# Optimization experiments

Measured on AMD Instinct MI355X. Metric: run time of the kernel, lower is better.

## Reference

```python
import jax, jax.numpy as jnp
import numpy as np

N = 100000       # nodes
E0 = 1600000     # edges without self loops
E = E0 + N       # with self loops appended (attr 0), matching add_self_loops
DIN = 128        # input_dim
HID = 64         # nb_hidden_gnn (per-head out_channels)
HEADS = 4
EMB = 128
L = 3            # nb_layer
NEG_SLOPE = 0.2
BN_EPS = 1e-5


def setup_inputs() -> dict:
    key = jax.random.key(0)
    ks = jax.random.split(key, 12)
    # edges with no self loops; self loops (i,i) appended with edge_attr 0
    row = jax.random.randint(ks[0], (E0,), 0, N)
    off = jax.random.randint(ks[1], (E0,), 1, N)
    col = (row + off) % N
    loops = jnp.arange(N, dtype=row.dtype)
    edge_index = jnp.stack([jnp.concatenate([row, loops]),
                            jnp.concatenate([col, loops])])
    edge_attr = jnp.concatenate([jax.random.normal(ks[2], (E0, 1), jnp.float32),
                                 jnp.zeros((N, 1), jnp.float32)])
    x = jax.random.normal(ks[3], (N, DIN), jnp.float32)
    HC = HEADS * HID
    linN0 = jax.random.normal(ks[4], (DIN, HC)) * HC ** -0.5
    linN_rest = jax.random.normal(ks[5], (L - 1, HID, HC)) * HC ** -0.5
    linE_all = jax.random.normal(ks[6], (L, 1, HEADS)) * HEADS ** -0.5  # nb_edge_attr=1
    att_all = jax.random.normal(ks[7], (L, HEADS, 2 * HID + 1)) * (2 * HID + 1) ** -0.5
    bias_all = jnp.zeros((L, HID))  # concat=False -> bias [out_channels]
    bn_gamma = jnp.ones((L - 1, HID))
    bn_beta = jnp.zeros((L - 1, HID))
    W = jax.random.normal(ks[8], (HID, EMB)) * HID ** -0.5
    b = jnp.zeros((EMB,))
    return {"x": x, "edge_index": edge_index, "edge_attr": edge_attr,
            "linN0": linN0, "linN_rest": linN_rest, "linE_all": linE_all,
            "att_all": att_all, "bias_all": bias_all,
            "bn_gamma": bn_gamma, "bn_beta": bn_beta, "W": W, "b": b}


def _gcn_layer(x, row, col, edge_attr, linN, linE, att, bias, bn):
    n = x.shape[0]
    if bn is not None:
        gamma, beta = bn
        mu = x.mean(axis=0)
        var = x.var(axis=0)
        x = (x - mu) * jax.lax.rsqrt(var + BN_EPS) * gamma + beta
    h = (x @ linN).reshape(n, HEADS, HID)                 # [N,H,C]
    e = (edge_attr @ linE)                                # [E,H] (nb_edge_attr=1)
    att_i = att[:, :HID]                                  # [H,C]
    att_j = att[:, HID:2 * HID]                           # [H,C]
    att_e = att[:, 2 * HID:]                              # [H,1]
    # per-node partial scores avoid gathering full features twice
    s_i = jnp.einsum('nhc,hc->nh', h, att_i)
    s_j = jnp.einsum('nhc,hc->nh', h, att_j)
    logits = s_i[row] + s_j[col] + e * att_e[:, 0]        # [E,H]
    logits = jax.nn.leaky_relu(logits, NEG_SLOPE)
    # segment softmax over destination nodes (edge_index[1])
    m = jax.ops.segment_max(logits, col, num_segments=n)
    p = jnp.exp(logits - m[col])
    denom = jax.ops.segment_sum(p, col, num_segments=n)
    alpha = p / (denom[col] + 1e-16)
    # message: alpha * x[source], scatter-add to destination
    msg = alpha[:, :, None] * h[row]                      # [E,H,C]
    out = jax.ops.segment_sum(msg, col, num_segments=n)   # [N,H,C]
    out = out.mean(axis=1) + bias + h.mean(axis=1)        # concat=False, res=True
    return jax.nn.relu(out)


def reference(x, edge_index, edge_attr, linN0, linN_rest, linE_all, att_all,
              bias_all, bn_gamma, bn_beta, W, b):
    row, col = edge_index[0], edge_index[1]
    emb = x
    for l in range(L):
        linN = linN0 if l == 0 else linN_rest[l - 1]
        bn = None if l == 0 else (bn_gamma[l - 1], bn_beta[l - 1])
        emb = _gcn_layer(emb, row, col, edge_attr, linN, linE_all[l],
                         att_all[l], bias_all[l], bn)
    return emb @ W + b
```

## Files before the change

### kernel.cpp

```cpp
#include <hip/hip_runtime.h>
#include <math.h>

#define NN 100000
#define E0E 1600000
#define EE (E0E + NN)
#define NEG 0.2f
#define BNEPS 1e-5f
#define LOG2E 1.4426950408889634f

typedef float f4 __attribute__((ext_vector_type(4)));
typedef float f2 __attribute__((ext_vector_type(2)));
typedef short s8v __attribute__((ext_vector_type(8)));

__device__ __forceinline__ float wred_max(float v) {
#pragma unroll
  for (int m = 1; m < 64; m <<= 1) v = fmaxf(v, __shfl_xor(v, m, 64));
  return v;
}
__device__ __forceinline__ float wred_sum(float v) {
#pragma unroll
  for (int m = 1; m < 64; m <<= 1) v += __shfl_xor(v, m, 64);
  return v;
}
__device__ __forceinline__ float sel4(float a0, float a1, float a2, float a3, int hd) {
  return (hd & 2) ? ((hd & 1) ? a3 : a2) : ((hd & 1) ? a1 : a0);
}
__device__ __forceinline__ unsigned short f2bf(float x) {
  unsigned u = __float_as_uint(x);
  return (unsigned short)((u + 0x7fffu + ((u >> 16) & 1u)) >> 16);
}
__device__ __forceinline__ float bf2f(unsigned short s) {
  return __uint_as_float(((unsigned)s) << 16);
}

__global__ void k_zero_i32(int* p, int n) {
  int i = blockIdx.x * blockDim.x + threadIdx.x;
  if (i < n) p[i] = 0;
}
__global__ void k_zero_f64(double* p, int n) {
  int i = blockIdx.x * blockDim.x + threadIdx.x;
  if (i < n) p[i] = 0.0;
}
__global__ void k_count(const int* __restrict__ col, int* cnt, int e) {
  int i = blockIdx.x * blockDim.x + threadIdx.x;
  if (i < e) atomicAdd(&cnt[col[i]], 1);
}
#define SCAN_T 1024
__global__ void k_scan1(const int* __restrict__ cnt, int* partial, int n, int chunk) {
  int i = blockIdx.x * blockDim.x + threadIdx.x;
  int beg = i * chunk, end = min(n, beg + chunk);
  int s = 0;
  for (int j = beg; j < end; ++j) s += cnt[j];
  partial[i] = s;
}
__global__ void k_scan2(int* partial) {
  __shared__ int lds[SCAN_T];
  int t = threadIdx.x;
  int v = partial[t];
  lds[t] = v;
  __syncthreads();
  for (int off = 1; off < SCAN_T; off <<= 1) {
    int add = (t >= off) ? lds[t - off] : 0;
    __syncthreads();
    lds[t] += add;
    __syncthreads();
  }
  partial[t] = lds[t] - v;
}
__global__ void k_scan3(const int* __restrict__ cnt, const int* __restrict__ partial,
                        int* rowptr, int* cursor, int n, int chunk, int etot) {
  int i = blockIdx.x * blockDim.x + threadIdx.x;
  int beg = i * chunk, end = min(n, beg + chunk);
  int run = partial[i];
  for (int j = beg; j < end; ++j) {
    rowptr[j] = run;
    cursor[j] = run;
    run += cnt[j];
  }
  if (i == SCAN_T - 1) rowptr[n] = etot;
}
__global__ void k_scatter(const int* __restrict__ row, const int* __restrict__ col,
                          const float* __restrict__ ea, int* cursor, int2* csr, int e) {
  int i = blockIdx.x * blockDim.x + threadIdx.x;
  if (i < e) {
    int c = col[i];
    int p = atomicAdd(&cursor[c], 1);
    csr[p] = make_int2(row[i], __float_as_int(ea[i]));
  }
}

__global__ void k_bnstats(const float* __restrict__ x, double* sums, int n) {
  int f = threadIdx.x & 63;
  int rt = (blockIdx.x * blockDim.x + threadIdx.x) >> 6;
  int rstride = (gridDim.x * blockDim.x) >> 6;
  double s = 0.0, q = 0.0;
  for (int r = rt; r < n; r += rstride) {
    double v = (double)x[(size_t)r * 64 + f];
    s += v;
    q += v * v;
  }
  __shared__ double ls[256], lq[256];
  ls[threadIdx.x] = s;
  lq[threadIdx.x] = q;
  __syncthreads();
  if (threadIdx.x < 64) {
    s = ls[threadIdx.x] + ls[threadIdx.x + 64] + ls[threadIdx.x + 128] + ls[threadIdx.x + 192];
    q = lq[threadIdx.x] + lq[threadIdx.x + 64] + lq[threadIdx.x + 128] + lq[threadIdx.x + 192];
    atomicAdd(&sums[f], s);
    atomicAdd(&sums[64 + f], q);
  }
}
__global__ void k_bnfinal(const double* __restrict__ sums, const float* __restrict__ gamma,
                          const float* __restrict__ beta, float* AB, int n) {
  int f = threadIdx.x;
  if (f < 64) {
    double mean = sums[f] / n;
    double var = sums[64 + f] / n - mean * mean;
    float A = gamma[f] * rsqrtf((float)var + BNEPS);
    AB[f] = A;
    AB[64 + f] = beta[f] - (float)mean * A;
  }
}

__global__ void k_prepw(const float* __restrict__ W, const float* __restrict__ AB,
                        const float* __restrict__ bin, unsigned short* __restrict__ Wt,
                        float* __restrict__ cvec, int K, int N, int mode) {
  int n = threadIdx.x;
  if (n >= N) return;
  float c = (mode == 2) ? bin[n] : 0.f;
  for (int k = 0; k < K; ++k) {
    float w = W[k * N + n];
    float a = 1.f, b = 0.f;
    if (mode == 1) { a = AB[k]; b = AB[64 + k]; }
    Wt[n * K + k] = f2bf(a * w);
    c = fmaf(b, w, c);
  }
  cvec[n] = c;
}

template <int K, int CT, bool ATT, bool OB>
__global__ __launch_bounds__(256, 2) void k_gemm(const float* __restrict__ x,
                                                 const unsigned short* __restrict__ Wt,
                                                 const float* __restrict__ cvec,
                                                 const float* __restrict__ att,
                                                 void* __restrict__ houtv,
                                                 float* __restrict__ s_i,
                                                 float* __restrict__ s_j, int n,
                                                 int ntiles) {
  constexpr int KS = K / 32;
  constexpr int ROWB = 2 * K;
  constexpr int CPR = K / 8;
  constexpr int NCOL = 4 * CT * 16;
  __shared__ unsigned char xs[64 * ROWB];
  const int lane = threadIdx.x & 63;
  const int wv = threadIdx.x >> 6;
  const int l15 = lane & 15;
  const int lq = lane >> 4;
  const int colbase = wv * CT * 16;

  s8v wfr[CT][KS];
#pragma unroll
  for (int ct = 0; ct < CT; ++ct)
#pragma unroll
    for (int ks = 0; ks < KS; ++ks)
      wfr[ct][ks] = *(const s8v*)&Wt[(size_t)(colbase + ct * 16 + l15) * K + ks * 32 + lq * 8];
  float cb[CT][4];
#pragma unroll
  for (int ct = 0; ct < CT; ++ct)
#pragma unroll
    for (int r = 0; r < 4; ++r) cb[ct][r] = cvec[colbase + ct * 16 + lq * 4 + r];
  float ati[ATT ? CT : 1][4], atj[ATT ? CT : 1][4];
  if constexpr (ATT) {
    const float* ar = att + wv * 129;
#pragma unroll
    for (int ct = 0; ct < CT; ++ct)
#pragma unroll
      for (int r = 0; r < 4; ++r) {
        int cc = ct * 16 + lq * 4 + r;
        ati[ct][r] = ar[cc];
        atj[ct][r] = ar[64 + cc];
      }
  }

  for (int t = blockIdx.x; t < ntiles; t += gridDim.x) {
    const int row0 = t * 64;
    __syncthreads();
#pragma unroll
    for (int i = 0; i < (64 * CPR) / 256; ++i) {
      int c = threadIdx.x + i * 256;
      int row = c / CPR, kc = c % CPR;
      int rg = min(row0 + row, n - 1);
      const float* xp = x + (size_t)rg * K + kc * 8;
      f4 a0 = *(const f4*)xp;
      f4 a1 = *(const f4*)(xp + 4);
      union { s8v v; unsigned short u[8]; } pk;
      pk.u[0] = f2bf(a0[0]); pk.u[1] = f2bf(a0[1]); pk.u[2] = f2bf(a0[2]); pk.u[3] = f2bf(a0[3]);
      pk.u[4] = f2bf(a1[0]); pk.u[5] = f2bf(a1[1]); pk.u[6] = f2bf(a1[2]); pk.u[7] = f2bf(a1[3]);
      *(s8v*)&xs[row * ROWB + ((kc * 16) ^ ((row & 7) << 4))] = pk.v;
    }
    __syncthreads();
    f4 acc[4][CT];
#pragma unroll
    for (int rt = 0; rt < 4; ++rt)
#pragma unroll
      for (int ct = 0; ct < CT; ++ct) acc[rt][ct] = (f4)0.f;
#pragma unroll
    for (int ks = 0; ks < KS; ++ks) {
      s8v xf[4];
#pragma unroll
      for (int rt = 0; rt < 4; ++rt) {
        int row = rt * 16 + l15;
        int kb = ks * 64 + lq * 16;
        xf[rt] = *(const s8v*)&xs[row * ROWB + (kb ^ ((row & 7) << 4))];
      }
#pragma unroll
      for (int rt = 0; rt < 4; ++rt)
#pragma unroll
        for (int ct = 0; ct < CT; ++ct)
          acc[rt][ct] = __builtin_amdgcn_mfma_f32_16x16x32_bf16(wfr[ct][ks], xf[rt],
                                                                acc[rt][ct], 0, 0, 0);
    }
#pragma unroll
    for (int rt = 0; rt < 4; ++rt) {
      if (row0 + rt * 16 >= n) continue;
      const size_t xrow = (size_t)(row0 + rt * 16 + l15);
      float v[CT][4];
#pragma unroll
      for (int ct = 0; ct < CT; ++ct)
#pragma unroll
        for (int r = 0; r < 4; ++r) v[ct][r] = acc[rt][ct][r] + cb[ct][r];
      if constexpr (OB) {
        float* outp = (float*)houtv;
#pragma unroll
        for (int ct = 0; ct < CT; ++ct) {
          f4 o;
          o[0] = v[ct][0]; o[1] = v[ct][1]; o[2] = v[ct][2]; o[3] = v[ct][3];
          *(f4*)&outp[xrow * NCOL + colbase + ct * 16 + lq * 4] = o;
        }
      } else {
        unsigned short* hout = (unsigned short*)houtv;
#pragma unroll
        for (int ct = 0; ct < CT; ++ct) {
          ushort4 hb4;
          hb4.x = f2bf(v[ct][0]); hb4.y = f2bf(v[ct][1]);
          hb4.z = f2bf(v[ct][2]); hb4.w = f2bf(v[ct][3]);
          *(ushort4*)&hout[xrow * NCOL + colbase + ct * 16 + lq * 4] = hb4;
        }
      }
      if constexpr (ATT) {
        float pi = 0.f, pj = 0.f;
#pragma unroll
        for (int ct = 0; ct < CT; ++ct)
#pragma unroll
          for (int r = 0; r < 4; ++r) {
            pi = fmaf(v[ct][r], ati[ct][r], pi);
            pj = fmaf(v[ct][r], atj[ct][r], pj);
          }
        pi += __shfl_xor(pi, 16, 64); pi += __shfl_xor(pi, 32, 64);
        pj += __shfl_xor(pj, 16, 64); pj += __shfl_xor(pj, 32, 64);
        if (lane < 16) {
          s_i[xrow * 4 + wv] = pi;
          s_j[xrow * 4 + wv] = pj;
        }
      }
    }
  }
}

__global__ __launch_bounds__(256) void k_edge(const int* __restrict__ rowptr,
                                              const int2* __restrict__ csr,
                                              const float* __restrict__ s_i,
                                              const float* __restrict__ s_j,
                                              const unsigned short* __restrict__ hb,
                                              const float* __restrict__ linE,
                                              const float* __restrict__ att,
                                              const float* __restrict__ bias,
                                              float* __restrict__ xout, int n) {
  __shared__ float lp[4][64][4];
  __shared__ int lsrc[4][64];
  const int lane = threadIdx.x & 63;
  const int wid = threadIdx.x >> 6;
  int v = blockIdx.x * 4 + wid;
  if (v >= n) return;
  v = __builtin_amdgcn_readfirstlane(v);
  const int base = rowptr[v];
  const int deg = rowptr[v + 1] - base;

  const float coef0 = linE[0] * att[0 * 129 + 128];
  const float coef1 = linE[1] * att[1 * 129 + 128];
  const float coef2 = linE[2] * att[2 * 129 + 128];
  const float coef3 = linE[3] * att[3 * 129 + 128];
  const float sj0 = s_j[(size_t)v * 4 + 0];
  const float sj1 = s_j[(size_t)v * 4 + 1];
  const float sj2 = s_j[(size_t)v * 4 + 2];
  const float sj3 = s_j[(size_t)v * 4 + 3];

  auto edge_logits = [&](int i, int& src, float& g0, float& g1, float& g2, float& g3) {
    int2 pk = csr[i];
    src = pk.x;
    float ea = __int_as_float(pk.y);
    f4 siv = *(const f4*)&s_i[(size_t)src * 4];
    g0 = siv[0] + sj0 + ea * coef0; g0 = fmaxf(g0, g0 * NEG);
    g1 = siv[1] + sj1 + ea * coef1; g1 = fmaxf(g1, g1 * NEG);
    g2 = siv[2] + sj2 + ea * coef2; g2 = fmaxf(g2, g2 * NEG);
    g3 = siv[3] + sj3 + ea * coef3; g3 = fmaxf(g3, g3 * NEG);
  };

  const int hd = lane >> 4;
  float msel, rdsel;
  bool fast = (deg <= 64);
  if (fast) {
    float g0 = -INFINITY, g1 = -INFINITY, g2 = -INFINITY, g3 = -INFINITY;
    int src = 0;
    bool valid = lane < deg;
    if (valid) edge_logits(base + lane, src, g0, g1, g2, g3);
    float m0 = wred_max(g0), m1 = wred_max(g1), m2 = wred_max(g2), m3 = wred_max(g3);
    float p0 = valid ? exp2f((g0 - m0) * LOG2E) : 0.f;
    float p1 = valid ? exp2f((g1 - m1) * LOG2E) : 0.f;
    float p2 = valid ? exp2f((g2 - m2) * LOG2E) : 0.f;
    float p3 = valid ? exp2f((g3 - m3) * LOG2E) : 0.f;
    if (valid) {
      f4 pp; pp[0] = p0; pp[1] = p1; pp[2] = p2; pp[3] = p3;
      *(f4*)&lp[wid][lane][0] = pp;
      lsrc[wid][lane] = src;
    }
    float d0 = wred_sum(p0), d1 = wred_sum(p1), d2 = wred_sum(p2), d3 = wred_sum(p3);
    rdsel = 1.f / (sel4(d0, d1, d2, d3, hd) + 1e-16f);
    msel = 0.f;
  } else {
    float m0 = -INFINITY, m1 = -INFINITY, m2 = -INFINITY, m3 = -INFINITY;
    for (int c0 = 0; c0 < deg; c0 += 64) {
      int i = c0 + lane;
      if (i < deg) {
        int src; float g0, g1, g2, g3;
        edge_logits(base + i, src, g0, g1, g2, g3);
        m0 = fmaxf(m0, g0); m1 = fmaxf(m1, g1); m2 = fmaxf(m2, g2); m3 = fmaxf(m3, g3);
      }
    }
    m0 = wred_max(m0); m1 = wred_max(m1); m2 = wred_max(m2); m3 = wred_max(m3);
    float d0 = 0, d1 = 0, d2 = 0, d3 = 0;
    for (int c0 = 0; c0 < deg; c0 += 64) {
      int i = c0 + lane;
      if (i < deg) {
        int src; float g0, g1, g2, g3;
        edge_logits(base + i, src, g0, g1, g2, g3);
        d0 += exp2f((g0 - m0) * LOG2E);
        d1 += exp2f((g1 - m1) * LOG2E);
        d2 += exp2f((g2 - m2) * LOG2E);
        d3 += exp2f((g3 - m3) * LOG2E);
      }
    }
    d0 = wred_sum(d0); d1 = wred_sum(d1); d2 = wred_sum(d2); d3 = wred_sum(d3);
    msel = sel4(m0, m1, m2, m3, hd);
    rdsel = 1.f / (sel4(d0, d1, d2, d3, hd) + 1e-16f);
  }

  f4 acc;
  {
    ushort4 hr = *(const ushort4*)&hb[(size_t)v * 256 + lane * 4];
    acc[0] = bf2f(hr.x); acc[1] = bf2f(hr.y); acc[2] = bf2f(hr.z); acc[3] = bf2f(hr.w);
  }
  if (fast) {
    for (int e = 0; e < deg; ++e) {
      int src = lsrc[wid][e];
      float a = lp[wid][e][hd] * rdsel;
      ushort4 hr = *(const ushort4*)&hb[(size_t)src * 256 + lane * 4];
      acc[0] = fmaf(a, bf2f(hr.x), acc[0]);
      acc[1] = fmaf(a, bf2f(hr.y), acc[1]);
      acc[2] = fmaf(a, bf2f(hr.z), acc[2]);
      acc[3] = fmaf(a, bf2f(hr.w), acc[3]);
    }
  } else {
    const float sjsel = sel4(sj0, sj1, sj2, sj3, hd);
    const float cfsel = sel4(coef0, coef1, coef2, coef3, hd);
    for (int e = base; e < base + deg; ++e) {
      int2 pk = csr[e];
      int src = pk.x;
      float ea = __int_as_float(pk.y);
      f4 siv = *(const f4*)&s_i[(size_t)src * 4];
      float lg = sel4(siv[0], siv[1], siv[2], siv[3], hd) + sjsel + ea * cfsel;
      lg = fmaxf(lg, lg * NEG);
      float a = exp2f((lg - msel) * LOG2E) * rdsel;
      ushort4 hr = *(const ushort4*)&hb[(size_t)src * 256 + lane * 4];
      acc[0] = fmaf(a, bf2f(hr.x), acc[0]);
      acc[1] = fmaf(a, bf2f(hr.y), acc[1]);
      acc[2] = fmaf(a, bf2f(hr.z), acc[2]);
      acc[3] = fmaf(a, bf2f(hr.w), acc[3]);
    }
  }
#pragma unroll
  for (int m = 16; m < 64; m <<= 1) {
    acc[0] += __shfl_xor(acc[0], m, 64);
    acc[1] += __shfl_xor(acc[1], m, 64);
    acc[2] += __shfl_xor(acc[2], m, 64);
    acc[3] += __shfl_xor(acc[3], m, 64);
  }
  if (lane < 16) {
    f4 bv = *(const f4*)&bias[lane * 4];
    f4 o;
#pragma unroll
    for (int c = 0; c < 4; ++c) o[c] = fmaxf(acc[c] * 0.25f + bv[c], 0.f);
    *(f4*)&xout[(size_t)v * 64 + lane * 4] = o;
  }
}

extern "C" void kernel_launch(void* const* d_in, const int* in_sizes, int n_in,
                              void* d_out, int out_size, void* d_ws, size_t ws_size,
                              hipStream_t stream) {
  const float* x_in = (const float*)d_in[0];
  const int* ei = (const int*)d_in[1];
  const float* eattr = (const float*)d_in[2];
  const float* linN0 = (const float*)d_in[3];
  const float* linNr = (const float*)d_in[4];
  const float* linE = (const float*)d_in[5];
  const float* attA = (const float*)d_in[6];
  const float* biasA = (const float*)d_in[7];
  const float* bng = (const float*)d_in[8];
  const float* bnb = (const float*)d_in[9];
  const float* W = (const float*)d_in[10];
  const float* bb = (const float*)d_in[11];
  float* out = (float*)d_out;

  const int* row = ei;
  const int* col = ei + EE;

  char* ws = (char*)d_ws;
  size_t o = 0;
  auto alloc = [&](size_t bytes) {
    void* p = ws + o;
    o += (bytes + 255) & ~(size_t)255;
    return p;
  };
  int* cnt = (int*)alloc((size_t)NN * 4);
  int* cursor = (int*)alloc((size_t)NN * 4);
  int* rowptr = (int*)alloc((size_t)(NN + 1) * 4);
  int* partial = (int*)alloc((size_t)SCAN_T * 4);
  int2* csr = (int2*)alloc((size_t)EE * 8);
  unsigned short* h = (unsigned short*)alloc((size_t)NN * 256 * 2);
  float* si = (float*)alloc((size_t)NN * 4 * 4);
  float* sj = (float*)alloc((size_t)NN * 4 * 4);
  float* xa = (float*)alloc((size_t)NN * 64 * 4);
  float* xb = (float*)alloc((size_t)NN * 64 * 4);
  double* bnsum = (double*)alloc(256 * 8);
  float* AB = (float*)alloc(128 * 4);
  unsigned short* Wt = (unsigned short*)alloc((size_t)256 * 128 * 2);
  float* cvec = (float*)alloc(256 * 4);
  if (o > ws_size) return;

  const int chunk = (NN + SCAN_T - 1) / SCAN_T;
  const int NTILES = (NN + 63) / 64;
  const int GG = 521;

  k_zero_i32<<<(NN + 255) / 256, 256, 0, stream>>>(cnt, NN);
  k_zero_f64<<<1, 256, 0, stream>>>(bnsum, 256);
  k_count<<<(EE + 255) / 256, 256, 0, stream>>>(col, cnt, EE);
  k_scan1<<<4, 256, 0, stream>>>(cnt, partial, NN, chunk);
  k_scan2<<<1, SCAN_T, 0, stream>>>(partial);
  k_scan3<<<4, 256, 0, stream>>>(cnt, partial, rowptr, cursor, NN, chunk, EE);
  k_scatter<<<(EE + 255) / 256, 256, 0, stream>>>(row, col, eattr, cursor, csr, EE);

  k_prepw<<<1, 256, 0, stream>>>(linN0, nullptr, nullptr, Wt, cvec, 128, 256, 0);
  k_gemm<128, 4, true, false><<<GG, 256, 0, stream>>>(x_in, Wt, cvec, attA + 0, h, si, sj,
                                                      NN, NTILES);
  k_edge<<<NN / 4, 256, 0, stream>>>(rowptr, csr, si, sj, h, linE + 0, attA + 0, biasA + 0, xa, NN);

  k_bnstats<<<256, 256, 0, stream>>>(xa, bnsum, NN);
  k_bnfinal<<<1, 64, 0, stream>>>(bnsum, bng + 0, bnb + 0, AB, NN);
  k_prepw<<<1, 256, 0, stream>>>(linNr, AB, nullptr, Wt, cvec, 64, 256, 1);
  k_gemm<64, 4, true, false><<<GG, 256, 0, stream>>>(xa, Wt, cvec, attA + 516, h, si, sj,
                                                     NN, NTILES);
  k_edge<<<NN / 4, 256, 0, stream>>>(rowptr, csr, si, sj, h, linE + 4, attA + 516, biasA + 64, xb, NN);

  k_bnstats<<<256, 256, 0, stream>>>(xb, bnsum + 128, NN);
  k_bnfinal<<<1, 64, 0, stream>>>(bnsum + 128, bng + 64, bnb + 64, AB, NN);
  k_prepw<<<1, 256, 0, stream>>>(linNr + 64 * 256, AB, nullptr, Wt, cvec, 64, 256, 1);
  k_gemm<64, 4, true, false><<<GG, 256, 0, stream>>>(xb, Wt, cvec, attA + 2 * 516, h, si, sj,
                                                     NN, NTILES);
  k_edge<<<NN / 4, 256, 0, stream>>>(rowptr, csr, si, sj, h, linE + 8, attA + 2 * 516, biasA + 128, xa, NN);

  k_prepw<<<1, 256, 0, stream>>>(W, nullptr, bb, Wt, cvec, 64, 128, 2);
  k_gemm<64, 2, false, true><<<GG, 256, 0, stream>>>(xa, Wt, cvec, nullptr, out, nullptr,
                                                     nullptr, NN, NTILES);
}
```

Before: 940.1 us.

## Merge init and BN-finalize kernels, unroll edge gather, launch one block per tile

Folds the two zeroing kernels into one init kernel and moves the batch-norm finalize into the weight-prep kernel, dropping three launches per forward. The fast-path message gather in the edge kernel is templated on an unroll factor so several neighbour feature rows are fetched before their FMAs. Each layer uses a different factor (4, 2, 1), which looks like an experiment. GEMM grids now launch one block per 64-row tile instead of a fixed 521 blocks.

```diff
diff --git a/kernel.cpp b/kernel.cpp
--- a/kernel.cpp
+++ b/kernel.cpp
@@ -33,13 +33,10 @@
   return __uint_as_float(((unsigned)s) << 16);
 }
 
-__global__ void k_zero_i32(int* p, int n) {
+__global__ void k_init(int* cnt, double* bnsum, int n) {
   int i = blockIdx.x * blockDim.x + threadIdx.x;
-  if (i < n) p[i] = 0;
-}
-__global__ void k_zero_f64(double* p, int n) {
-  int i = blockIdx.x * blockDim.x + threadIdx.x;
-  if (i < n) p[i] = 0.0;
+  if (i < n) cnt[i] = 0;
+  if (i < 256) bnsum[i] = 0.0;
 }
 __global__ void k_count(const int* __restrict__ col, int* cnt, int e) {
   int i = blockIdx.x * blockDim.x + threadIdx.x;
@@ -110,32 +107,33 @@
     atomicAdd(&sums[64 + f], q);
   }
 }
-__global__ void k_bnfinal(const double* __restrict__ sums, const float* __restrict__ gamma,
-                          const float* __restrict__ beta, float* AB, int n) {
-  int f = threadIdx.x;
-  if (f < 64) {
-    double mean = sums[f] / n;
-    double var = sums[64 + f] / n - mean * mean;
-    float A = gamma[f] * rsqrtf((float)var + BNEPS);
-    AB[f] = A;
-    AB[64 + f] = beta[f] - (float)mean * A;
-  }
-}
-
-__global__ void k_prepw(const float* __restrict__ W, const float* __restrict__ AB,
+
+__global__ void k_prepw(const float* __restrict__ W, const double* __restrict__ bnsum,
+                        const float* __restrict__ gamma, const float* __restrict__ beta,
                         const float* __restrict__ bin, unsigned short* __restrict__ Wt,
                         float* __restrict__ cvec, int K, int N, int mode) {
-  int n = threadIdx.x;
-  if (n >= N) return;
-  float c = (mode == 2) ? bin[n] : 0.f;
+  __shared__ float ABl[128];
+  int t = threadIdx.x;
+  if (mode == 1) {
+    if (t < 64) {
+      double mean = bnsum[t] / NN;
+      double var = bnsum[64 + t] / NN - mean * mean;
+      float A = gamma[t] * rsqrtf((float)var + BNEPS);
+      ABl[t] = A;
+      ABl[64 + t] = beta[t] - (float)mean * A;
+    }
+    __syncthreads();
+  }
+  if (t >= N) return;
+  float c = (mode == 2) ? bin[t] : 0.f;
   for (int k = 0; k < K; ++k) {
-    float w = W[k * N + n];
+    float w = W[k * N + t];
     float a = 1.f, b = 0.f;
-    if (mode == 1) { a = AB[k]; b = AB[64 + k]; }
-    Wt[n * K + k] = f2bf(a * w);
+    if (mode == 1) { a = ABl[k]; b = ABl[64 + k]; }
+    Wt[t * K + k] = f2bf(a * w);
     c = fmaf(b, w, c);
   }
-  cvec[n] = c;
+  cvec[t] = c;
 }
 
 template <int K, int CT, bool ATT, bool OB>
@@ -267,6 +265,7 @@
   }
 }
 
+template <int UNR>
 __global__ __launch_bounds__(256) void k_edge(const int* __restrict__ rowptr,
                                               const int2* __restrict__ csr,
                                               const float* __restrict__ s_i,
@@ -361,14 +360,37 @@
     acc[0] = bf2f(hr.x); acc[1] = bf2f(hr.y); acc[2] = bf2f(hr.z); acc[3] = bf2f(hr.w);
   }
   if (fast) {
-    for (int e = 0; e < deg; ++e) {
-      int src = lsrc[wid][e];
-      float a = lp[wid][e][hd] * rdsel;
-      ushort4 hr = *(const ushort4*)&hb[(size_t)src * 256 + lane * 4];
-      acc[0] = fmaf(a, bf2f(hr.x), acc[0]);
-      acc[1] = fmaf(a, bf2f(hr.y), acc[1]);
-      acc[2] = fmaf(a, bf2f(hr.z), acc[2]);
-      acc[3] = fmaf(a, bf2f(hr.w), acc[3]);
+    int e = 0;
+    if constexpr (UNR > 1) {
+      for (; e + UNR <= deg; e += UNR) {
+        int ss[UNR];
+        float aa[UNR];
+        ushort4 hh[UNR];
+#pragma unroll
+        for (int u = 0; u < UNR; ++u) {
+          ss[u] = lsrc[wid][e + u];
+          aa[u] = lp[wid][e + u][hd] * rdsel;
+        }
+#pragma unroll
+        for (int u = 0; u < UNR; ++u)
+          hh[u] = *(const ushort4*)&hb[(size_t)ss[u] * 256 + lane * 4];
+#pragma unroll
+        for (int u = 0; u < UNR; ++u) {
+          acc[0] = fmaf(aa[u], bf2f(hh[u].x), acc[0]);
+          acc[1] = fmaf(aa[u], bf2f(hh[u].y), acc[1]);
+          acc[2] = fmaf(aa[u], bf2f(hh[u].z), acc[2]);
+          acc[3] = fmaf(aa[u], bf2f(hh[u].w), acc[3]);
+        }
+      }
+    }
+    for (; e < deg; ++e) {
+      int s0 = lsrc[wid][e];
+      float a0 = lp[wid][e][hd] * rdsel;
+      ushort4 h0 = *(const ushort4*)&hb[(size_t)s0 * 256 + lane * 4];
+      acc[0] = fmaf(a0, bf2f(h0.x), acc[0]);
+      acc[1] = fmaf(a0, bf2f(h0.y), acc[1]);
+      acc[2] = fmaf(a0, bf2f(h0.z), acc[2]);
+      acc[3] = fmaf(a0, bf2f(h0.w), acc[3]);
     }
   } else {
     const float sjsel = sel4(sj0, sj1, sj2, sj3, hd);
@@ -442,43 +464,42 @@
   float* xa = (float*)alloc((size_t)NN * 64 * 4);
   float* xb = (float*)alloc((size_t)NN * 64 * 4);
   double* bnsum = (double*)alloc(256 * 8);
-  float* AB = (float*)alloc(128 * 4);
   unsigned short* Wt = (unsigned short*)alloc((size_t)256 * 128 * 2);
   float* cvec = (float*)alloc(256 * 4);
   if (o > ws_size) return;
 
   const int chunk = (NN + SCAN_T - 1) / SCAN_T;
   const int NTILES = (NN + 63) / 64;
-  const int GG = 521;
-
-  k_zero_i32<<<(NN + 255) / 256, 256, 0, stream>>>(cnt, NN);
-  k_zero_f64<<<1, 256, 0, stream>>>(bnsum, 256);
+
+  k_init<<<(NN + 255) / 256, 256, 0, stream>>>(cnt, bnsum, NN);
   k_count<<<(EE + 255) / 256, 256, 0, stream>>>(col, cnt, EE);
   k_scan1<<<4, 256, 0, stream>>>(cnt, partial, NN, chunk);
   k_scan2<<<1, SCAN_T, 0, stream>>>(partial);
   k_scan3<<<4, 256, 0, stream>>>(cnt, partial, rowptr, cursor, NN, chunk, EE);
   k_scatter<<<(EE + 255) / 256, 256, 0, stream>>>(row, col, eattr, cursor, csr, EE);
 
-  k_prepw<<<1, 256, 0, stream>>>(linN0, nullptr, nullptr, Wt, cvec, 128, 256, 0);
-  k_gemm<128, 4, true, false><<<GG, 256, 0, stream>>>(x_in, Wt, cvec, attA + 0, h, si, sj,
-                                                      NN, NTILES);
-  k_edge<<<NN / 4, 256, 0, stream>>>(rowptr, csr, si, sj, h, linE + 0, attA + 0, biasA + 0, xa, NN);
+  k_prepw<<<1, 256, 0, stream>>>(linN0, nullptr, nullptr, nullptr, nullptr, Wt, cvec, 128, 256, 0);
+  k_gemm<128, 4, true, false><<<NTILES, 256, 0, stream>>>(x_in, Wt, cvec, attA + 0, h, si, sj,
+                                                          NN, NTILES);
+  k_edge<4><<<NN / 4, 256, 0, stream>>>(rowptr, csr, si, sj, h, linE + 0, attA + 0, biasA + 0,
+                                        xa, NN);
 
   k_bnstats<<<256, 256, 0, stream>>>(xa, bnsum, NN);
-  k_bnfinal<<<1, 64, 0, stream>>>(bnsum, bng + 0, bnb + 0, AB, NN);
-  k_prepw<<<1, 256, 0, stream>>>(linNr, AB, nullptr, Wt, cvec, 64, 256, 1);
-  k_gemm<64, 4, true, false><<<GG, 256, 0, stream>>>(xa, Wt, cvec, attA + 516, h, si, sj,
-                                                     NN, NTILES);
-  k_edge<<<NN / 4, 256, 0, stream>>>(rowptr, csr, si, sj, h, linE + 4, attA + 516, biasA + 64, xb, NN);
+  k_prepw<<<1, 256, 0, stream>>>(linNr, bnsum, bng, bnb, nullptr, Wt, cvec, 64, 256, 1);
+  k_gemm<64, 4, true, false><<<NTILES, 256, 0, stream>>>(xa, Wt, cvec, attA + 516, h, si, sj,
+                                                         NN, NTILES);
+  k_edge<2><<<NN / 4, 256, 0, stream>>>(rowptr, csr, si, sj, h, linE + 4, attA + 516, biasA + 64,
+                                        xb, NN);
 
   k_bnstats<<<256, 256, 0, stream>>>(xb, bnsum + 128, NN);
-  k_bnfinal<<<1, 64, 0, stream>>>(bnsum + 128, bng + 64, bnb + 64, AB, NN);
-  k_prepw<<<1, 256, 0, stream>>>(linNr + 64 * 256, AB, nullptr, Wt, cvec, 64, 256, 1);
-  k_gemm<64, 4, true, false><<<GG, 256, 0, stream>>>(xb, Wt, cvec, attA + 2 * 516, h, si, sj,
-                                                     NN, NTILES);
-  k_edge<<<NN / 4, 256, 0, stream>>>(rowptr, csr, si, sj, h, linE + 8, attA + 2 * 516, biasA + 128, xa, NN);
-
-  k_prepw<<<1, 256, 0, stream>>>(W, nullptr, bb, Wt, cvec, 64, 128, 2);
-  k_gemm<64, 2, false, true><<<GG, 256, 0, stream>>>(xa, Wt, cvec, nullptr, out, nullptr,
-                                                     nullptr, NN, NTILES);
-}
+  k_prepw<<<1, 256, 0, stream>>>(linNr + 64 * 256, bnsum + 128, bng + 64, bnb + 64, nullptr,
+                                 Wt, cvec, 64, 256, 1);
+  k_gemm<64, 4, true, false><<<NTILES, 256, 0, stream>>>(xb, Wt, cvec, attA + 2 * 516, h, si, sj,
+                                                         NN, NTILES);
+  k_edge<1><<<NN / 4, 256, 0, stream>>>(rowptr, csr, si, sj, h, linE + 8, attA + 2 * 516,
+                                        biasA + 128, xa, NN);
+
+  k_prepw<<<1, 256, 0, stream>>>(W, nullptr, nullptr, nullptr, bb, Wt, cvec, 64, 128, 2);
+  k_gemm<64, 2, false, true><<<NTILES, 256, 0, stream>>>(xa, Wt, cvec, nullptr, out, nullptr,
+                                                         nullptr, NN, NTILES);
+}
```

Result: faster. 904.6 us (-3.8%).
